# Optimization experiments

Hardware: AMD Instinct MI355X
Metric: run time of the kernel (lower is better)

The kernel has to match this reference:

```python
import jax, jax.numpy as jnp
import numpy as np

H = 16          # n_head
N = 64          # head_size
LN_EPS = 1e-5 * 8.0 ** 2  # eps * head_size_divisor**2


def _group_norm(x, w, b):
    # x: (B*T, C), H groups of size N, biased variance (torch GroupNorm)
    BT, C = x.shape
    xg = x.reshape(BT, H, C // H)
    m = xg.mean(-1, keepdims=True)
    v = xg.var(-1, keepdims=True)
    xn = (xg - m) / jnp.sqrt(v + LN_EPS)
    return xn.reshape(BT, C) * w + b


def _rwkv7(r, w, k, v, a, b):
    # RWKV-7: S_t = S_{t-1} * diag(exp(-exp(w_t))) + (S_{t-1} a_t) b_t^T + v_t k_t^T ; y_t = S_t r_t
    B, T, C = r.shape
    def rs(z):
        return z.reshape(B, T, H, N).transpose(1, 0, 2, 3)  # (T,B,H,N)
    wd = jnp.exp(-jnp.exp(rs(w)))
    xs = (rs(r), wd, rs(k), rs(v), rs(a), rs(b))
    def step(S, inp):
        rt, wt, kt, vt, at, bt = inp  # each (B,H,N)
        sa = jnp.einsum('bhij,bhj->bhi', S, at)
        S = S * wt[:, :, None, :] + sa[..., None] * bt[:, :, None, :] + vt[..., None] * kt[:, :, None, :]
        return S, jnp.einsum('bhij,bhj->bhi', S, rt)
    S0 = jnp.zeros((B, H, N, N), r.dtype)
    _, y = jax.lax.scan(step, S0, xs)
    return y.transpose(1, 0, 2, 3).reshape(B, T, C)


def setup_inputs():
    key = jax.random.key(0)
    B, T, C = 2, 2048, 1024
    ks = iter(jax.random.split(key, 32))
    def p(shape, s):
        return jax.random.normal(next(ks), shape, jnp.float32) * s
    return {
        'x': p((B, T, C), 1.0),
        'time_maa_x': p((1, 1, C), 0.5), 'time_maa_r': p((1, 1, C), 0.5),
        'time_maa_w': p((1, 1, C), 0.5), 'time_maa_k': p((1, 1, C), 0.5),
        'time_maa_v': p((1, 1, C), 0.5), 'time_maa_a': p((1, 1, C), 0.5),
        'time_maa_g': p((1, 1, C), 0.5),
        'time_decay': p((1, 1, C), 1.0),
        'time_faaaa': p((H, N), 0.1),
        'time_aaaaa': p((1, 1, C), 0.1),
        'time_maa_w1': p((C, 192), 0.02), 'time_maa_w2': p((6, 32, C), 0.02),
        'time_decay_w1': p((C, 64), 0.02), 'time_decay_w2': p((64, C), 0.1),
        'time_aaa_w1': p((C, 64), 0.02), 'time_aaa_w2': p((64, C), 0.1),
        'time_kkk_w1': p((C, 64), 0.02), 'time_kkk_w2': p((64, C), 0.1),
        'gate_w1': p((C, 128), 0.02), 'gate_w2': p((128, C), 0.1),
        'W_r': p((C, C), 0.03), 'W_k': p((C, C), 0.03),
        'W_v': p((C, C), 0.03), 'W_o': p((C, C), 0.03),
        'ln_w': jnp.ones((C,), jnp.float32), 'ln_b': jnp.zeros((C,), jnp.float32),
    }


def reference(x, time_maa_x, time_maa_r, time_maa_w, time_maa_k, time_maa_v,
              time_maa_a, time_maa_g, time_decay, time_faaaa, time_aaaaa,
              time_maa_w1, time_maa_w2, time_decay_w1, time_decay_w2,
              time_aaa_w1, time_aaa_w2, time_kkk_w1, time_kkk_w2,
              gate_w1, gate_w2, W_r, W_k, W_v, W_o, ln_w, ln_b):
    B, T, C = x.shape
    # time_shift: xx[t] = x[t-1] - x[t], x[-1] = 0
    xx = jnp.pad(x, ((0, 0), (1, 0), (0, 0)))[:, :T] - x
    # low-rank token-mix interpolation coefficients (6 branches)
    mix = jnp.tanh((x + xx * time_maa_x) @ time_maa_w1).reshape(B, T, 6, -1)
    m = jnp.einsum('btsd,sdc->sbtc', mix, time_maa_w2)  # (6,B,T,C)
    mr, mw, mk, mv, ma, mg = m[0], m[1], m[2], m[3], m[4], m[5]
    xr = x + xx * (time_maa_r + mr)
    xw = x + xx * (time_maa_w + mw)
    xk = x + xx * (time_maa_k + mk)
    xv = x + xx * (time_maa_v + mv)
    xa = x + xx * (time_maa_a + ma)
    xg = x + xx * (time_maa_g + mg)
    r = xr @ W_r
    w = -jax.nn.softplus(-(time_decay + jnp.tanh(xw @ time_decay_w1) @ time_decay_w2)) - 0.5
    k = xk @ W_k
    v = xv @ W_v
    g = jnp.tanh(xg @ gate_w1) @ gate_w2
    kk = k + jnp.tanh(xk @ time_kkk_w1) @ time_kkk_w2
    kk = kk / jnp.maximum(jnp.linalg.norm(kk, axis=-1, keepdims=True), 1e-12)
    a = jax.nn.sigmoid(time_aaaaa + (xa @ time_aaa_w1) @ time_aaa_w2) * 2.0
    k = k * jnp.exp(jnp.minimum(w * 0.5, 0.0))
    y = _rwkv7(r, w, k, v, -kk, kk * a)
    y = _group_norm(y.reshape(B * T, C), ln_w, ln_b).reshape(B, T, C)
    rh = r.reshape(B, T, H, N)
    kh = k.reshape(B, T, H, N)
    vh = v.reshape(B, T, H, N)
    bonus = ((rh * kh * time_faaaa).sum(-1, keepdims=True) * vh).reshape(B, T, C)
    y = y + bonus
    return (y * g) @ W_o
```

## Files before the change

### kernel.cpp

```cpp
#include <hip/hip_runtime.h>
#include <hip/hip_bf16.h>

using bf16 = __hip_bfloat16;
using bf16x8 = __attribute__((ext_vector_type(8))) short;
using f32x4 = __attribute__((ext_vector_type(4))) float;

#define B_ 2
#define T_ 2048
#define C_ 1024
#define BT_ (B_*T_)
#define H_ 16
#define N_ 64
#define LCH 32
#define NCH (T_/LCH)
#define CHD (B_*H_*NCH)

__device__ __forceinline__ float allred64(float v) {
#pragma unroll
  for (int m = 1; m < 64; m <<= 1) v += __shfl_xor(v, m, 64);
  return v;
}

__device__ __forceinline__ bf16 tobf(float f) { return __float2bfloat16(f); }
__device__ __forceinline__ float frombf(bf16 b) { return __bfloat162float(b); }
__device__ __forceinline__ float bf2f(unsigned short u) {
  unsigned int x = ((unsigned int)u) << 16;
  return __builtin_bit_cast(float, x);
}
__device__ __forceinline__ unsigned short bfbits(float f) {
  return __builtin_bit_cast(unsigned short, __float2bfloat16(f));
}
__device__ __forceinline__ float rdlane(float v, int m) {
  return __builtin_bit_cast(float,
      __builtin_amdgcn_readlane(__builtin_bit_cast(int, v), m));
}

__device__ __forceinline__ f32x4 mfma16x16x32(bf16x8 a, bf16x8 b, f32x4 c) {
  return __builtin_amdgcn_mfma_f32_16x16x32_bf16(a, b, c, 0, 0, 0);
}

typedef const __attribute__((address_space(1))) unsigned int* gas_ptr;
typedef __attribute__((address_space(3))) unsigned int* las_ptr;
__device__ __forceinline__ void gload16(const void* g, void* l) {
  __builtin_amdgcn_global_load_lds((gas_ptr)g, (las_ptr)l, 16, 0, 0);
}

__global__ void ws_diag(float a, float b, float* out) { out[0] = a; out[1] = b; }

struct PrepArgs {
  const float* src[19];
  bf16* dst[19];
};
__constant__ int kTR[19] = {1024,1024,1024,1024, 1024, 32,32,32,32,32,32,
                            1024,64, 1024,64, 1024,64, 1024,128};
__constant__ int kTC[19] = {1024,1024,1024,1024, 192, 1024,1024,1024,1024,1024,1024,
                            64,1024, 64,1024, 64,1024, 128,1024};

__global__ __launch_bounds__(256) void prep_weights(PrepArgs pa) {
  const int job = blockIdx.y;
  const int R = kTR[job], Cc = kTC[job];
  const int ntx = Cc >> 5, nty = R >> 5;
  const int tile = blockIdx.x;
  if (tile >= ntx * nty) return;
  const int tx = tile % ntx, ty = tile / ntx;
  const float* __restrict__ src = pa.src[job];
  bf16* __restrict__ dst = pa.dst[job];
  __shared__ float tl[32][33];
  const int lx = threadIdx.x & 31, ly = threadIdx.x >> 5;
#pragma unroll
  for (int q = 0; q < 4; ++q)
    tl[ly + 8*q][lx] = src[(size_t)(ty*32 + ly + 8*q) * Cc + tx*32 + lx];
  __syncthreads();
#pragma unroll
  for (int q = 0; q < 4; ++q)
    dst[(size_t)(tx*32 + ly + 8*q) * R + ty*32 + lx] = tobf(tl[lx][ly + 8*q]);
}

template<int EPI>
__global__ __launch_bounds__(256) void gemm_bt(
    const bf16* __restrict__ A, int lda,
    const bf16* __restrict__ Bt, int ldb,
    void* __restrict__ Cout, int ldc, int K)
{
  __shared__ short As[64][40];
  __shared__ short Bs[64][40];
  const int bm0 = blockIdx.x * 64;
  const int bn0 = blockIdx.y * 64;
  const int tid = threadIdx.x;
  const int wave = tid >> 6, lane = tid & 63;
  const int lm = lane & 15, kg = lane >> 4;
  const int srow = tid >> 2, scol = (tid & 3) * 8;
  f32x4 acc[4] = {};
  const size_t abase = (size_t)(bm0 + srow) * lda + scol;
  const size_t bbase = (size_t)(bn0 + srow) * ldb + scol;
  for (int k0 = 0; k0 < K; k0 += 32) {
    *(uint4*)&As[srow][scol] = *(const uint4*)(A + abase + k0);
    *(uint4*)&Bs[srow][scol] = *(const uint4*)(Bt + bbase + k0);
    __syncthreads();
    bf16x8 af = *(const bf16x8*)&As[wave*16 + lm][kg*8];
#pragma unroll
    for (int f = 0; f < 4; ++f) {
      bf16x8 bfr = *(const bf16x8*)&Bs[f*16 + lm][kg*8];
      acc[f] = mfma16x16x32(af, bfr, acc[f]);
    }
    __syncthreads();
  }
  const int row0 = bm0 + wave*16 + kg*4;
  const int col0 = bn0 + lm;
#pragma unroll
  for (int f = 0; f < 4; ++f) {
#pragma unroll
    for (int q = 0; q < 4; ++q) {
      float val = acc[f][q];
      size_t o = (size_t)(row0 + q) * ldc + col0 + f*16;
      if (EPI == 0)      ((float*)Cout)[o] = val;
      else if (EPI == 1) ((bf16*)Cout)[o] = tobf(tanhf(val));
      else               ((bf16*)Cout)[o] = tobf(val);
    }
  }
}

struct Proj4Args { const bf16* A[4]; const bf16* Bt[4]; bf16* out[4];
                   int N[4]; int tnh[4]; };
__global__ __launch_bounds__(256) void proj4(Proj4Args p4) {
  const int z = blockIdx.z;
  const int Nn = p4.N[z];
  const int bn0 = blockIdx.y * 64;
  if (bn0 >= Nn) return;
  __shared__ short As[64][40];
  __shared__ short Bs[64][40];
  const bf16* __restrict__ A  = p4.A[z];
  const bf16* __restrict__ Bt = p4.Bt[z];
  bf16* __restrict__ out = p4.out[z];
  const int tnh = p4.tnh[z];
  const int bm0 = blockIdx.x * 64;
  const int tid = threadIdx.x;
  const int wave = tid >> 6, lane = tid & 63;
  const int lm = lane & 15, kg = lane >> 4;
  const int srow = tid >> 2, scol = (tid & 3) * 8;
  f32x4 acc[4] = {};
  const size_t abase = (size_t)(bm0 + srow) * C_ + scol;
  const size_t bbase = (size_t)(bn0 + srow) * C_ + scol;
  for (int k0 = 0; k0 < C_; k0 += 32) {
    *(uint4*)&As[srow][scol] = *(const uint4*)(A + abase + k0);
    *(uint4*)&Bs[srow][scol] = *(const uint4*)(Bt + bbase + k0);
    __syncthreads();
    bf16x8 af = *(const bf16x8*)&As[wave*16 + lm][kg*8];
#pragma unroll
    for (int f = 0; f < 4; ++f) {
      bf16x8 bfr = *(const bf16x8*)&Bs[f*16 + lm][kg*8];
      acc[f] = mfma16x16x32(af, bfr, acc[f]);
    }
    __syncthreads();
  }
  const int row0 = bm0 + wave*16 + kg*4;
  const int col0 = bn0 + lm;
#pragma unroll
  for (int f = 0; f < 4; ++f) {
#pragma unroll
    for (int q = 0; q < 4; ++q) {
      float val = acc[f][q];
      size_t o = (size_t)(row0 + q) * Nn + col0 + f*16;
      out[o] = tobf(tnh ? tanhf(val) : val);
    }
  }
}

template<int EPI>
__global__ __launch_bounds__(256) void gemm128(
    const bf16* __restrict__ A, int lda,
    const bf16* __restrict__ Bt, int ldb,
    void* __restrict__ Cout, int ldc, int K,
    const float* __restrict__ aux1, bf16* __restrict__ aux2)
{
  __shared__ bf16 As[128][32];
  __shared__ bf16 Bs[128][32];
  const int bm0 = blockIdx.x * 128, bn0 = blockIdx.y * 128;
  const int tid = threadIdx.x, wv = tid >> 6, ln = tid & 63;
  const int wr = wv >> 1, wc = wv & 1;
  const int lm = ln & 15, kg = ln >> 4;
  const int srow = ln >> 2, scol = (ln & 3) * 8;
  f32x4 acc[4][4] = {};
  for (int k0 = 0; k0 < K; k0 += 32) {
#pragma unroll
    for (int i = 0; i < 2; ++i) {
      const int r0 = wv*32 + i*16;
      gload16(A  + (size_t)(bm0 + r0 + srow) * lda + k0 + scol, &As[r0][0]);
      gload16(Bt + (size_t)(bn0 + r0 + srow) * ldb + k0 + scol, &Bs[r0][0]);
    }
    asm volatile("s_waitcnt vmcnt(0)" ::: "memory");
    __syncthreads();
    bf16x8 af[4], bfr[4];
#pragma unroll
    for (int m = 0; m < 4; ++m) af[m] = *(const bf16x8*)&As[wr*64 + m*16 + lm][kg*8];
#pragma unroll
    for (int n = 0; n < 4; ++n) bfr[n] = *(const bf16x8*)&Bs[wc*64 + n*16 + lm][kg*8];
#pragma unroll
    for (int m = 0; m < 4; ++m)
#pragma unroll
      for (int n = 0; n < 4; ++n)
        acc[m][n] = mfma16x16x32(af[m], bfr[n], acc[m][n]);
    __syncthreads();
  }
#pragma unroll
  for (int m = 0; m < 4; ++m) {
    const int row0 = bm0 + wr*64 + m*16 + kg*4;
#pragma unroll
    for (int n = 0; n < 4; ++n) {
      const int col = bn0 + wc*64 + n*16 + lm;
#pragma unroll
      for (int q = 0; q < 4; ++q) {
        float val = acc[m][n][q];
        size_t o = (size_t)(row0 + q) * ldc + col;
        if (EPI == 0)      ((float*)Cout)[o] = val;
        else if (EPI == 2) ((bf16*)Cout)[o] = tobf(val);
        else if (EPI == 3) {
          float wr2 = val + aux1[col];
          float sp = fmaxf(-wr2, 0.f) + log1pf(expf(-fabsf(wr2)));
          float w = -sp - 0.5f;
          ((bf16*)Cout)[o] = tobf(-expf(w));
          aux2[o] = tobf(frombf(aux2[o]) * expf(fminf(0.5f*w, 0.f)));
        } else if (EPI == 4) {
          float z = aux1[col] + val;
          ((bf16*)Cout)[o] = tobf(2.f / (1.f + expf(-z)));
        }
      }
    }
  }
}

struct RkvArgs { const bf16* A[3]; const bf16* Bt[3]; bf16* Cq[3]; };
__global__ __launch_bounds__(256) void gemm128_rkv(RkvArgs ra) {
  __shared__ bf16 As[128][32];
  __shared__ bf16 Bs[128][32];
  const bf16* __restrict__ A  = ra.A[blockIdx.z];
  const bf16* __restrict__ Bt = ra.Bt[blockIdx.z];
  bf16* __restrict__ Cout = ra.Cq[blockIdx.z];
  const int bm0 = blockIdx.x * 128, bn0 = blockIdx.y * 128;
  const int tid = threadIdx.x, wv = tid >> 6, ln = tid & 63;
  const int wr = wv >> 1, wc = wv & 1;
  const int lm = ln & 15, kg = ln >> 4;
  const int srow = ln >> 2, scol = (ln & 3) * 8;
  f32x4 acc[4][4] = {};
  for (int k0 = 0; k0 < C_; k0 += 32) {
#pragma unroll
    for (int i = 0; i < 2; ++i) {
      const int r0 = wv*32 + i*16;
      gload16(A  + (size_t)(bm0 + r0 + srow) * C_ + k0 + scol, &As[r0][0]);
      gload16(Bt + (size_t)(bn0 + r0 + srow) * C_ + k0 + scol, &Bs[r0][0]);
    }
    asm volatile("s_waitcnt vmcnt(0)" ::: "memory");
    __syncthreads();
    bf16x8 af[4], bfr[4];
#pragma unroll
    for (int m = 0; m < 4; ++m) af[m] = *(const bf16x8*)&As[wr*64 + m*16 + lm][kg*8];
#pragma unroll
    for (int n = 0; n < 4; ++n) bfr[n] = *(const bf16x8*)&Bs[wc*64 + n*16 + lm][kg*8];
#pragma unroll
    for (int m = 0; m < 4; ++m)
#pragma unroll
      for (int n = 0; n < 4; ++n)
        acc[m][n] = mfma16x16x32(af[m], bfr[n], acc[m][n]);
    __syncthreads();
  }
#pragma unroll
  for (int m = 0; m < 4; ++m) {
    const int row0 = bm0 + wr*64 + m*16 + kg*4;
#pragma unroll
    for (int n = 0; n < 4; ++n) {
      const int col = bn0 + wc*64 + n*16 + lm;
#pragma unroll
      for (int q = 0; q < 4; ++q)
        Cout[(size_t)(row0 + q) * C_ + col] = tobf(acc[m][n][q]);
    }
  }
}

struct Mix6Args { const float* maa[6]; bf16* out[6]; };

__global__ __launch_bounds__(256) void mix_combine(
    const bf16* __restrict__ mixb, const bf16* __restrict__ w2t,
    const bf16* __restrict__ xb, Mix6Args ma)
{
  __shared__ short As[64][40];
  __shared__ short Bs[64][40];
  const int s6 = blockIdx.z;
  const bf16* __restrict__ A  = mixb + s6*32;
  const bf16* __restrict__ Bt = w2t + (size_t)s6*C_*32;
  const float* __restrict__ maa = ma.maa[s6];
  bf16* __restrict__ out = ma.out[s6];
  const int bm0 = blockIdx.x * 64, bn0 = blockIdx.y * 64;
  const int tid = threadIdx.x, wave = tid >> 6, lane = tid & 63;
  const int lm = lane & 15, kg = lane >> 4;
  const int srow = tid >> 2, scol = (tid & 3) * 8;
  *(uint4*)&As[srow][scol] = *(const uint4*)(A + (size_t)(bm0 + srow)*192 + scol);
  *(uint4*)&Bs[srow][scol] = *(const uint4*)(Bt + (size_t)(bn0 + srow)*32 + scol);
  __syncthreads();
  bf16x8 af = *(const bf16x8*)&As[wave*16 + lm][kg*8];
  f32x4 acc[4] = {};
#pragma unroll
  for (int f = 0; f < 4; ++f) {
    bf16x8 bfr = *(const bf16x8*)&Bs[f*16 + lm][kg*8];
    acc[f] = mfma16x16x32(af, bfr, acc[f]);
  }
  const int row0 = bm0 + wave*16 + kg*4;
  const int col0 = bn0 + lm;
#pragma unroll
  for (int f = 0; f < 4; ++f) {
#pragma unroll
    for (int q = 0; q < 4; ++q) {
      const int row = row0 + q, col = col0 + f*16;
      const size_t o = (size_t)row * C_ + col;
      float xv = frombf(xb[o]);
      float xp = (row & (T_ - 1)) ? frombf(xb[o - C_]) : 0.f;
      out[o] = tobf(xv + (xp - xv) * (maa[col] + acc[f][q]));
    }
  }
}

__global__ __launch_bounds__(256) void xin_k(
    const float* __restrict__ x, const float* __restrict__ maa_x,
    bf16* __restrict__ xinb, bf16* __restrict__ xb)
{
  size_t idx = (size_t)blockIdx.x * 256 + threadIdx.x;
  int c = idx & (C_ - 1);
  int t = (int)((idx >> 10) & (T_ - 1));
  float xv = x[idx];
  float xp = t ? x[idx - C_] : 0.f;
  xinb[idx] = tobf(xv + (xp - xv) * maa_x[c]);
  xb[idx] = tobf(xv);
}

__global__ __launch_bounds__(256) void kk_normalize(
    const bf16* __restrict__ kraw, const bf16* __restrict__ kkadd,
    bf16* __restrict__ kkout)
{
  const int bt = blockIdx.x;
  const int tid = threadIdx.x;
  const size_t o = (size_t)bt * C_;
  float vals[4]; float ss = 0.f;
#pragma unroll
  for (int q = 0; q < 4; ++q) {
    float u = frombf(kraw[o + tid + q*256]) + frombf(kkadd[o + tid + q*256]);
    vals[q] = u; ss += u * u;
  }
  ss = allred64(ss);
  __shared__ float red[4];
  const int wave = tid >> 6, lane = tid & 63;
  if (lane == 0) red[wave] = ss;
  __syncthreads();
  float tot = red[0] + red[1] + red[2] + red[3];
  float inv = 1.f / fmaxf(sqrtf(tot), 1e-12f);
#pragma unroll
  for (int q = 0; q < 4; ++q) kkout[o + tid + q*256] = tobf(vals[q] * inv);
}


__global__ __launch_bounds__(256, 3) void rwkv_chunk_pre(
    const bf16* __restrict__ rr, const bf16* __restrict__ lw,
    const bf16* __restrict__ kk_s, const bf16* __restrict__ kkv,
    const bf16* __restrict__ aam, const bf16* __restrict__ vv,
    bf16* __restrict__ wbufb, bf16* __restrict__ sabufb,
    bf16* __restrict__ abybufb, bf16* __restrict__ ckybufb,
    bf16* __restrict__ ubufP, bf16* __restrict__ mbufT)
{
  __shared__ float Am[LCH][33], Cm[LCH][33];
  __shared__ float wtot[4][64];
  __shared__ float lcl[64];
  __shared__ bf16 bTb[LCH][72], kTb[LCH][72], vLb[LCH][72];
  __shared__ bf16 bTT[64][40], kTT[64][40], vLT[64][40];
  __shared__ bf16 uni[5120];
  bf16 (*aCb)[72] = (bf16(*)[72])uni;
  bf16 (*rCb)[72] = (bf16(*)[72])(uni + 2304);
  bf16 (*WT)[40]  = (bf16(*)[40])uni;
  bf16 (*SAT)[40] = (bf16(*)[40])(uni + 2560);

  const int ch = blockIdx.x;
  const int c  = ch & (NCH - 1);
  const int bh = ch >> 6;
  const int b  = bh >> 4, h = bh & 15;
  const int tid = threadIdx.x, wv = tid >> 6, ln = tid & 63;
  const int lm = ln & 15, kg = ln >> 4;
  const size_t base = ((size_t)(b*T_ + c*LCH) * C_) + h*N_ + ln;

  float lwr[8], lcE[8];
  {
    float run = 0.f;
#pragma unroll
    for (int q = 0; q < 8; ++q) {
      lwr[q] = frombf(lw[base + (size_t)(wv*8 + q) * C_]);
      lcE[q] = run; run += lwr[q];
    }
    wtot[wv][ln] = run;
  }
  __syncthreads();
  {
    float pre = 0.f;
    for (int w2 = 0; w2 < wv; ++w2) pre += wtot[w2][ln];
    if (wv == 0) lcl[ln] = wtot[0][ln] + wtot[1][ln] + wtot[2][ln] + wtot[3][ln];
#pragma unroll
    for (int q = 0; q < 8; ++q) lcE[q] += pre;
  }
#pragma unroll
  for (int q = 0; q < 8; ++q) {
    const int s = wv*8 + q;
    const size_t off = base + (size_t)s * C_;
    float kkx = frombf(kkv[off]), aax = frombf(aam[off]);
    float kx = frombf(kk_s[off]), rx = frombf(rr[off]);
    float lcI = lcE[q] + lwr[q];
    float eIm = __expf(-lcI);
    float av = -kkx * __expf(lcE[q]);
    float bv = kkx * aax * eIm;
    float kv2 = kx * eIm;
    float rv = rx * __expf(lcI);
    bf16 vxb = vv[off];
    aCb[s][ln] = tobf(av);  rCb[s][ln] = tobf(rv);
    bTb[s][ln] = tobf(bv);  kTb[s][ln] = tobf(kv2);
    vLb[s][ln] = vxb;
    bTT[ln][s] = tobf(bv);  kTT[ln][s] = tobf(kv2);  vLT[ln][s] = vxb;
  }
  __syncthreads();

  {
    const bf16 (*Ab)[72] = (wv < 2) ? aCb : rCb;
    const bf16 (*Bb)[72] = (wv & 1) ? kTb : bTb;
#pragma unroll
    for (int mt = 0; mt < 2; ++mt)
#pragma unroll
      for (int nt = 0; nt < 2; ++nt) {
        f32x4 acc = {};
#pragma unroll
        for (int ks = 0; ks < 2; ++ks) {
          bf16x8 af = *(const bf16x8*)&Ab[mt*16 + lm][ks*32 + kg*8];
          bf16x8 bq = *(const bf16x8*)&Bb[nt*16 + lm][ks*32 + kg*8];
          acc = mfma16x16x32(af, bq, acc);
        }
        const int row0 = mt*16 + kg*4, col = nt*16 + lm;
#pragma unroll
        for (int q = 0; q < 4; ++q) {
          float v = acc[q];
          if (wv == 0)      Am[row0+q][col] = v;
          else if (wv == 1) Cm[row0+q][col] = v;
          else {
            bf16 bv2 = tobf(col <= row0+q ? v : 0.f);
            if (wv == 2) abybufb[(size_t)ch*1024 + (row0+q)*32 + col] = bv2;
            else         ckybufb[(size_t)ch*1024 + (row0+q)*32 + col] = bv2;
          }
        }
      }
  }
  __syncthreads();

  float Xr[32], amr[32];
  if (wv == 0) {
#pragma unroll
    for (int s = 0; s < 32; ++s) amr[s] = Am[s][ln & 31];
#pragma unroll
    for (int s = 0; s < 32; ++s) Xr[s] = frombf(aCb[s][ln]);
  } else if (wv == 1) {
    float cmr[32];
#pragma unroll
    for (int s = 0; s < 32; ++s) { amr[s] = Am[s][ln & 31]; cmr[s] = Cm[s][ln & 31]; }
#pragma unroll
    for (int s = 0; s < 32; ++s) Xr[s] = 0.f;
#pragma unroll
    for (int u = 0; u < 31; ++u) {
      float v = frombf(vLb[u][ln]);
#pragma unroll
      for (int s = u + 1; s < 32; ++s) Xr[s] += rdlane(cmr[s], u) * v;
    }
  }
  __syncthreads();

  if (wv < 2) {
#pragma unroll
    for (int s = 1; s < 32; ++s) {
      float acc = Xr[s];
#pragma unroll
      for (int u = 0; u < s; ++u) acc += rdlane(amr[s], u) * Xr[u];
      Xr[s] = acc;
    }
    if (wv == 0) {
#pragma unroll
      for (int s = 0; s < 32; ++s) {
        bf16 bv = tobf(Xr[s]);
        WT[ln][s] = bv;
        wbufb[(size_t)ch*2048 + s*64 + ln] = bv;
      }
    } else {
#pragma unroll
      for (int s = 0; s < 32; ++s) {
        bf16 bv = tobf(Xr[s]);
        SAT[ln][s] = bv;
        sabufb[(size_t)ch*2048 + s*64 + ln] = bv;
      }
    }
  }
  __syncthreads();

  {
    const int mt = wv;
    bf16x8 aS = *(const bf16x8*)&SAT[mt*16 + lm][kg*8];
    bf16x8 aV = *(const bf16x8*)&vLT[mt*16 + lm][kg*8];
    bf16x8 aW = *(const bf16x8*)&WT[mt*16 + lm][kg*8];
#pragma unroll
    for (int nt = 0; nt < 4; ++nt) {
      bf16x8 bB = *(const bf16x8*)&bTT[nt*16 + lm][kg*8];
      bf16x8 bK = *(const bf16x8*)&kTT[nt*16 + lm][kg*8];
      f32x4 aU = {}, aG = {};
      aU = mfma16x16x32(aS, bB, aU);
      aU = mfma16x16x32(aV, bK, aU);
      aG = mfma16x16x32(aW, bB, aG);
      const int i0r = mt*16 + kg*4, col = nt*16 + lm;
      float dl = __expf(lcl[col]);
      uint2 up;
      up.x = (unsigned int)bfbits(aU[0]*dl) | ((unsigned int)bfbits(aU[1]*dl) << 16);
      up.y = (unsigned int)bfbits(aU[2]*dl) | ((unsigned int)bfbits(aU[3]*dl) << 16);
      *(uint2*)(ubufP + (size_t)ch*4096 + (mt*4 + nt)*256 + ln*4) = up;
      float m0 = (aG[0] + (i0r+0 == col ? 1.f : 0.f)) * dl;
      float m1 = (aG[1] + (i0r+1 == col ? 1.f : 0.f)) * dl;
      float m2 = (aG[2] + (i0r+2 == col ? 1.f : 0.f)) * dl;
      float m3 = (aG[3] + (i0r+3 == col ? 1.f : 0.f)) * dl;
      uint2 mp;
      mp.x = (unsigned int)bfbits(m0) | ((unsigned int)bfbits(m1) << 16);
      mp.y = (unsigned int)bfbits(m2) | ((unsigned int)bfbits(m3) << 16);
      const int laned = (((mt*2) + (kg >> 1)) & 3) * 16 + lm;
      *(uint2*)(mbufT + (size_t)ch*4096 + (nt*2 + (mt >> 1))*512
                + laned*8 + (kg & 1)*4) = mp;
    }
  }
}

__global__ __launch_bounds__(256) void rwkv_chunk_state(
    const bf16* __restrict__ mbufT, const bf16* __restrict__ ubufP,
    bf16* __restrict__ s0bufb)
{
  __shared__ bf16 Sst[4][16][72];
  const int bh = blockIdx.x;
  const int tid = threadIdx.x, wv = tid >> 6, ln = tid & 63;
  const int lm = ln & 15, kg = ln >> 4;

#pragma unroll
  for (int r = 0; r < 16; ++r) {
    Sst[wv][r][ln] = tobf(0.f);
    if (ln < 8) Sst[wv][r][64 + ln] = tobf(0.f);
  }

  bf16x8 BfA[4][2], BfB[4][2];
  uint2 UpA[4], UpB[4];
  auto prefetch = [&](bf16x8 (&Bf)[4][2], uint2 (&Up)[4], int c) {
    const size_t chp = (size_t)(bh*NCH + c) * 4096;
#pragma unroll
    for (int nt = 0; nt < 4; ++nt) {
      Bf[nt][0] = *(const bf16x8*)(mbufT + chp + (nt*2 + 0)*512 + ln*8);
      Bf[nt][1] = *(const bf16x8*)(mbufT + chp + (nt*2 + 1)*512 + ln*8);
      Up[nt]    = *(const uint2*) (ubufP + chp + (wv*4 + nt)*256 + ln*4);
    }
  };
  prefetch(BfA, UpA, 0);
  prefetch(BfB, UpB, 1);

  auto body = [&](bf16x8 (&Bf)[4][2], uint2 (&Up)[4], int c) {
    const size_t ch4 = (size_t)(bh*NCH + c) * 4096;
    const int sr = ln >> 2, sc = (ln & 3) * 16;
    uint4 v0 = *(const uint4*)&Sst[wv][sr][sc];
    uint4 v1 = *(const uint4*)&Sst[wv][sr][sc + 8];
    *(uint4*)(s0bufb + ch4 + (size_t)(wv*16 + sr)*64 + sc) = v0;
    *(uint4*)(s0bufb + ch4 + (size_t)(wv*16 + sr)*64 + sc + 8) = v1;
    bf16x8 A0 = *(const bf16x8*)&Sst[wv][lm][kg*8];
    bf16x8 A1 = *(const bf16x8*)&Sst[wv][lm][32 + kg*8];
    f32x4 acc[4];
#pragma unroll
    for (int nt = 0; nt < 4; ++nt) {
      acc[nt][0] = bf2f((unsigned short)(Up[nt].x & 0xffff));
      acc[nt][1] = bf2f((unsigned short)(Up[nt].x >> 16));
      acc[nt][2] = bf2f((unsigned short)(Up[nt].y & 0xffff));
      acc[nt][3] = bf2f((unsigned short)(Up[nt].y >> 16));
      acc[nt] = mfma16x16x32(A0, Bf[nt][0], acc[nt]);
      acc[nt] = mfma16x16x32(A1, Bf[nt][1], acc[nt]);
    }
    int cp = c + 2; if (cp > NCH - 1) cp = NCH - 1;
    prefetch(Bf, Up, cp);
#pragma unroll
    for (int nt = 0; nt < 4; ++nt)
#pragma unroll
      for (int q = 0; q < 4; ++q)
        Sst[wv][kg*4 + q][nt*16 + lm] = tobf(acc[nt][q]);
  };

  for (int cc = 0; cc < NCH; cc += 2) {
    body(BfA, UpA, cc);
    body(BfB, UpB, cc + 1);
  }
}

__global__ __launch_bounds__(256, 4) void rwkv_chunk_out(
    const bf16* __restrict__ rr, const bf16* __restrict__ lw,
    const bf16* __restrict__ vv, const bf16* __restrict__ s0bufb,
    const bf16* __restrict__ wbufb, const bf16* __restrict__ sabufb,
    const bf16* __restrict__ abybufb, const bf16* __restrict__ ckybufb,
    float* __restrict__ y)
{
  __shared__ bf16 S0b[64][72];
  __shared__ bf16 Wb[LCH][72], Rlb[LCH][72];
  __shared__ bf16 ABl[LCH][40], CKl[LCH][40];
  __shared__ bf16 SAot[64][40], VlT[64][40];
  __shared__ float wtot[4][64];
  const int ch = blockIdx.x;
  const int c = ch & (NCH - 1), bh = ch >> 6, b = bh >> 4, h = bh & 15;
  const int tid = threadIdx.x, wv = tid >> 6, ln = tid & 63;
  const int lm = ln & 15, kg = ln >> 4;
  const size_t base = ((size_t)(b*T_ + c*LCH) * C_) + h*N_ + ln;

  float lwr[8], lcE[8];
  {
    float run = 0.f;
#pragma unroll
    for (int q = 0; q < 8; ++q) {
      lwr[q] = frombf(lw[base + (size_t)(wv*8 + q) * C_]);
      lcE[q] = run; run += lwr[q];
    }
    wtot[wv][ln] = run;
  }
  __syncthreads();
  {
    float pre = 0.f;
    for (int w2 = 0; w2 < wv; ++w2) pre += wtot[w2][ln];
#pragma unroll
    for (int q = 0; q < 8; ++q) lcE[q] += pre;
  }
#pragma unroll
  for (int q = 0; q < 8; ++q) {
    const int s = wv*8 + q;
    const size_t off = base + (size_t)s * C_;
    Rlb[s][ln] = tobf(frombf(rr[off]) * __expf(lcE[q] + lwr[q]));
    VlT[ln][s] = vv[off];
  }
#pragma unroll
  for (int t = 0; t < 2; ++t) {
    int cc2 = tid*2 + t; int ri = cc2 >> 3, co = (cc2 & 7) * 8;
    *(uint4*)&S0b[ri][co] = *(const uint4*)(s0bufb + (size_t)ch*4096 + ri*64 + co);
  }
  { int ri = tid >> 3, co = (tid & 7) * 8;
    *(uint4*)&Wb[ri][co] = *(const uint4*)(wbufb + (size_t)ch*2048 + ri*64 + co); }
  if (tid < 128) {
    int ri = tid >> 2, co = (tid & 3) * 8;
    *(uint4*)&ABl[ri][co] = *(const uint4*)(abybufb + (size_t)ch*1024 + ri*32 + co);
  } else {
    int t2 = tid - 128; int ri = t2 >> 2, co = (t2 & 3) * 8;
    *(uint4*)&CKl[ri][co] = *(const uint4*)(ckybufb + (size_t)ch*1024 + ri*32 + co);
  }
  __syncthreads();

  const int mt = wv >> 1, ntb = (wv & 1) * 2;
#pragma unroll
  for (int t = 0; t < 2; ++t) {
    const int nt = ntb + t;
    const int row0 = mt*16 + kg*4, col = nt*16 + lm;
    f32x4 acc;
#pragma unroll
    for (int q = 0; q < 4; ++q)
      acc[q] = frombf(sabufb[(size_t)ch*2048 + (row0+q)*64 + col]);
#pragma unroll
    for (int ks = 0; ks < 2; ++ks) {
      bf16x8 af = *(const bf16x8*)&Wb[mt*16 + lm][ks*32 + kg*8];
      bf16x8 bq = *(const bf16x8*)&S0b[nt*16 + lm][ks*32 + kg*8];
      acc = mfma16x16x32(af, bq, acc);
    }
#pragma unroll
    for (int q = 0; q < 4; ++q) SAot[col][row0+q] = tobf(acc[q]);
  }
  __syncthreads();

#pragma unroll
  for (int t = 0; t < 2; ++t) {
    const int nt = ntb + t;
    f32x4 acc = {};
#pragma unroll
    for (int ks = 0; ks < 2; ++ks) {
      bf16x8 af = *(const bf16x8*)&Rlb[mt*16 + lm][ks*32 + kg*8];
      bf16x8 bq = *(const bf16x8*)&S0b[nt*16 + lm][ks*32 + kg*8];
      acc = mfma16x16x32(af, bq, acc);
    }
    {
      bf16x8 af = *(const bf16x8*)&ABl[mt*16 + lm][kg*8];
      bf16x8 bq = *(const bf16x8*)&SAot[nt*16 + lm][kg*8];
      acc = mfma16x16x32(af, bq, acc);
    }
    {
      bf16x8 af = *(const bf16x8*)&CKl[mt*16 + lm][kg*8];
      bf16x8 bq = *(const bf16x8*)&VlT[nt*16 + lm][kg*8];
      acc = mfma16x16x32(af, bq, acc);
    }
    const int row0 = mt*16 + kg*4, col = nt*16 + lm;
#pragma unroll
    for (int q = 0; q < 4; ++q)
      y[((size_t)(b*T_ + c*LCH + row0 + q)) * C_ + h*N_ + col] = acc[q];
  }
}

__global__ __launch_bounds__(256) void gn_bonus_gate(
    const float* __restrict__ y, const bf16* __restrict__ rr,
    const bf16* __restrict__ kk_s, const bf16* __restrict__ vv,
    const bf16* __restrict__ gg, const float* __restrict__ faaaa,
    const float* __restrict__ lnw, const float* __restrict__ lnb,
    bf16* __restrict__ zb)
{
  const int bt = blockIdx.x;
  const int wave = threadIdx.x >> 6, lane = threadIdx.x & 63;
  const float inv64 = 1.f / 64.f;
  for (int h = wave; h < H_; h += 4) {
    const int c = h * 64 + lane;
    const size_t o = (size_t)bt * C_ + c;
    float yv = y[o];
    float mean = allred64(yv) * inv64;
    float d = yv - mean;
    float var = allred64(d * d) * inv64;
    float xn = d * rsqrtf(var + 6.4e-4f);
    float gn = xn * lnw[c] + lnb[c];
    float rk = allred64(frombf(rr[o]) * frombf(kk_s[o]) * faaaa[c]);
    float z = (gn + rk * frombf(vv[o])) * frombf(gg[o]);
    zb[o] = tobf(z);
  }
}

extern "C" void kernel_launch(void* const* d_in, const int* in_sizes, int n_in,
                              void* d_out, int out_size, void* d_ws, size_t ws_size,
                              hipStream_t stream)
{
  const float* x     = (const float*)d_in[0];
  const float* maa_x = (const float*)d_in[1];
  const float* maa_r = (const float*)d_in[2];
  const float* maa_w = (const float*)d_in[3];
  const float* maa_k = (const float*)d_in[4];
  const float* maa_v = (const float*)d_in[5];
  const float* maa_a = (const float*)d_in[6];
  const float* maa_g = (const float*)d_in[7];
  const float* tdec  = (const float*)d_in[8];
  const float* faaaa = (const float*)d_in[9];
  const float* aaaaa = (const float*)d_in[10];
  const float* maa_w1= (const float*)d_in[11];
  const float* maa_w2= (const float*)d_in[12];
  const float* dec_w1= (const float*)d_in[13];
  const float* dec_w2= (const float*)d_in[14];
  const float* aaa_w1= (const float*)d_in[15];
  const float* aaa_w2= (const float*)d_in[16];
  const float* kkk_w1= (const float*)d_in[17];
  const float* kkk_w2= (const float*)d_in[18];
  const float* gate_w1=(const float*)d_in[19];
  const float* gate_w2=(const float*)d_in[20];
  const float* W_r   = (const float*)d_in[21];
  const float* W_k   = (const float*)d_in[22];
  const float* W_v   = (const float*)d_in[23];
  const float* W_o   = (const float*)d_in[24];
  const float* lnw   = (const float*)d_in[25];
  const float* lnb   = (const float*)d_in[26];

  char* ws = (char*)d_ws;
  size_t cur = 0;
  auto alloc = [&](size_t bytes) -> void* {
    void* p = ws + cur; cur += (bytes + 255) & ~(size_t)255; return p;
  };
  const size_t HBT = (size_t)BT_ * C_ * 2;

  bf16* rb   = (bf16*)alloc(HBT);
  bf16* kb   = (bf16*)alloc(HBT);
  bf16* vb   = (bf16*)alloc(HBT);
  bf16* gbb  = (bf16*)alloc(HBT);
  bf16* WtR  = (bf16*)alloc((size_t)C_*C_*2);
  bf16* WtK  = (bf16*)alloc((size_t)C_*C_*2);
  bf16* WtV  = (bf16*)alloc((size_t)C_*C_*2);
  bf16* WtO  = (bf16*)alloc((size_t)C_*C_*2);
  bf16* w1t  = (bf16*)alloc((size_t)192*C_*2);
  bf16* w2t  = (bf16*)alloc((size_t)6*C_*32*2);
  bf16* d1t  = (bf16*)alloc((size_t)64*C_*2);
  bf16* d2t  = (bf16*)alloc((size_t)C_*64*2);
  bf16* a1t  = (bf16*)alloc((size_t)64*C_*2);
  bf16* a2t  = (bf16*)alloc((size_t)C_*64*2);
  bf16* k1t  = (bf16*)alloc((size_t)64*C_*2);
  bf16* k2t  = (bf16*)alloc((size_t)C_*64*2);
  bf16* g1t  = (bf16*)alloc((size_t)128*C_*2);
  bf16* g2t  = (bf16*)alloc((size_t)C_*128*2);
  bf16* lwb  = (bf16*)alloc(HBT);
  bf16* kkb  = (bf16*)alloc(HBT);
  bf16* aamt = (bf16*)alloc(HBT);
  bf16* s0bufb = kkb;

  const size_t ubase = cur;
  bf16* mtmpb = (bf16*)alloc(HBT);
  bf16* xinb = (bf16*)alloc(HBT);
  bf16* xb   = (bf16*)alloc(HBT);
  bf16* mixb = (bf16*)alloc((size_t)BT_*192*2);
  bf16* xbr[6];
  for (int s = 0; s < 6; ++s) xbr[s] = (bf16*)alloc(HBT);
  bf16* h64k = (bf16*)alloc((size_t)BT_*64*2);
  bf16* h64d = (bf16*)alloc((size_t)BT_*64*2);
  bf16* h64a = (bf16*)alloc((size_t)BT_*64*2);
  bf16* h128b= (bf16*)alloc((size_t)BT_*128*2);
  const size_t tmp_end = cur;
  cur = ubase;
  bf16*  wbufb   = (bf16*)alloc((size_t)CHD*2048*2);
  bf16*  sabufb  = (bf16*)alloc((size_t)CHD*2048*2);
  bf16*  abybufb = (bf16*)alloc((size_t)CHD*1024*2);
  bf16*  ckybufb = (bf16*)alloc((size_t)CHD*1024*2);
  bf16*  ubufP   = (bf16*)alloc((size_t)CHD*4096*2);
  bf16*  mbufT   = (bf16*)alloc((size_t)CHD*4096*2);
  bf16*  zb      = (bf16*)ubufP;
  if (tmp_end > cur) cur = tmp_end;
  const size_t need = cur;
  (void)in_sizes; (void)n_in; (void)out_size;

  if (ws_size < need) {
    ws_diag<<<1, 1, 0, stream>>>((float)ws_size, (float)need, (float*)d_out);
    return;
  }

  PrepArgs pa;
  pa.src[0] = W_r;  pa.dst[0] = WtR;
  pa.src[1] = W_k;  pa.dst[1] = WtK;
  pa.src[2] = W_v;  pa.dst[2] = WtV;
  pa.src[3] = W_o;  pa.dst[3] = WtO;
  pa.src[4] = maa_w1; pa.dst[4] = w1t;
  for (int s = 0; s < 6; ++s) { pa.src[5+s] = maa_w2 + (size_t)s*32*C_; pa.dst[5+s] = w2t + (size_t)s*C_*32; }
  pa.src[11] = dec_w1; pa.dst[11] = d1t;
  pa.src[12] = dec_w2; pa.dst[12] = d2t;
  pa.src[13] = aaa_w1; pa.dst[13] = a1t;
  pa.src[14] = aaa_w2; pa.dst[14] = a2t;
  pa.src[15] = kkk_w1; pa.dst[15] = k1t;
  pa.src[16] = kkk_w2; pa.dst[16] = k2t;
  pa.src[17] = gate_w1; pa.dst[17] = g1t;
  pa.src[18] = gate_w2; pa.dst[18] = g2t;
  prep_weights<<<dim3(1024, 19), 256, 0, stream>>>(pa);

  const int EW_GRID = (BT_ * C_) / 256;
  xin_k<<<EW_GRID, 256, 0, stream>>>(x, maa_x, xinb, xb);

  gemm_bt<1><<<dim3(64, 3), 256, 0, stream>>>(xinb, C_, w1t, C_, mixb, 192, C_);

  Mix6Args ma;
  ma.maa[0] = maa_r; ma.maa[1] = maa_w; ma.maa[2] = maa_k;
  ma.maa[3] = maa_v; ma.maa[4] = maa_a; ma.maa[5] = maa_g;
  for (int s = 0; s < 6; ++s) ma.out[s] = xbr[s];
  mix_combine<<<dim3(64, 16, 6), 256, 0, stream>>>(mixb, w2t, xb, ma);

  RkvArgs ra;
  ra.A[0] = xbr[0]; ra.Bt[0] = WtR; ra.Cq[0] = rb;
  ra.A[1] = xbr[2]; ra.Bt[1] = WtK; ra.Cq[1] = kb;
  ra.A[2] = xbr[3]; ra.Bt[2] = WtV; ra.Cq[2] = vb;
  gemm128_rkv<<<dim3(32, 8, 3), 256, 0, stream>>>(ra);

  Proj4Args p4;
  p4.A[0] = xbr[2]; p4.Bt[0] = k1t; p4.out[0] = h64k; p4.N[0] = 64;  p4.tnh[0] = 1;
  p4.A[1] = xbr[1]; p4.Bt[1] = d1t; p4.out[1] = h64d; p4.N[1] = 64;  p4.tnh[1] = 1;
  p4.A[2] = xbr[4]; p4.Bt[2] = a1t; p4.out[2] = h64a; p4.N[2] = 64;  p4.tnh[2] = 0;
  p4.A[3] = xbr[5]; p4.Bt[3] = g1t; p4.out[3] = h128b; p4.N[3] = 128; p4.tnh[3] = 1;
  proj4<<<dim3(64, 2, 4), 256, 0, stream>>>(p4);

  gemm128<2><<<dim3(32, 8), 256, 0, stream>>>(h64k, 64, k2t, 64, mtmpb, C_, 64, nullptr, nullptr);
  kk_normalize<<<BT_, 256, 0, stream>>>(kb, mtmpb, kkb);

  gemm128<3><<<dim3(32, 8), 256, 0, stream>>>(h64d, 64, d2t, 64, lwb, C_, 64, tdec, kb);

  gemm128<4><<<dim3(32, 8), 256, 0, stream>>>(h64a, 64, a2t, 64, aamt, C_, 64, aaaaa, nullptr);

  gemm128<2><<<dim3(32, 8), 256, 0, stream>>>(h128b, 128, g2t, 128, gbb, C_, 128, nullptr, nullptr);

  rwkv_chunk_pre<<<CHD, 256, 0, stream>>>(rb, lwb, kb, kkb, aamt, vb,
      wbufb, sabufb, abybufb, ckybufb, ubufP, mbufT);
  rwkv_chunk_state<<<32, 256, 0, stream>>>(mbufT, ubufP, s0bufb);
  rwkv_chunk_out<<<CHD, 256, 0, stream>>>(rb, lwb, vb, s0bufb, wbufb, sabufb,
      abybufb, ckybufb, (float*)d_out);

  gn_bonus_gate<<<BT_, 256, 0, stream>>>((const float*)d_out, rb, kb, vb, gbb,
                                         faaaa, lnw, lnb, zb);

  gemm128<0><<<dim3(32, 8), 256, 0, stream>>>(zb, C_, WtO, C_, d_out, C_, C_, nullptr, nullptr);
}
```

Measured before the change: 320.3 us.

## Fuse group norm, bonus and gating into chunk output kernel

The separate gn_bonus_gate kernel is folded into rwkv_chunk_out. The bonus term is reduced per timestep while r and k are loaded, and the MFMA output tile is staged in shared memory that reuses the Wb/Rlb buffers. Group norm, bonus and gate are then applied in the same block, which writes bf16 z directly. This removes a kernel launch and the fp32 y round trip through global memory, at the cost of extra syncs, more shared memory and a redundant duplicated epilogue loop.

```diff
diff --git a/kernel.cpp b/kernel.cpp
--- a/kernel.cpp
+++ b/kernel.cpp
@@ -596,16 +596,23 @@
 
 __global__ __launch_bounds__(256, 4) void rwkv_chunk_out(
     const bf16* __restrict__ rr, const bf16* __restrict__ lw,
-    const bf16* __restrict__ vv, const bf16* __restrict__ s0bufb,
+    const bf16* __restrict__ vv, const bf16* __restrict__ kks,
+    const bf16* __restrict__ gg, const bf16* __restrict__ s0bufb,
     const bf16* __restrict__ wbufb, const bf16* __restrict__ sabufb,
     const bf16* __restrict__ abybufb, const bf16* __restrict__ ckybufb,
-    float* __restrict__ y)
+    const float* __restrict__ faaaa, const float* __restrict__ lnw,
+    const float* __restrict__ lnb, bf16* __restrict__ zb)
 {
   __shared__ bf16 S0b[64][72];
-  __shared__ bf16 Wb[LCH][72], Rlb[LCH][72];
   __shared__ bf16 ABl[LCH][40], CKl[LCH][40];
   __shared__ bf16 SAot[64][40], VlT[64][40];
   __shared__ float wtot[4][64];
+  __shared__ float bonus[LCH];
+  __shared__ float uni2f[2304];
+  bf16 (*Wb)[72]  = (bf16(*)[72])uni2f;
+  bf16 (*Rlb)[72] = (bf16(*)[72])((bf16*)uni2f + 2304);
+  float (*Yl)[68] = (float(*)[68])uni2f;
+
   const int ch = blockIdx.x;
   const int c = ch & (NCH - 1), bh = ch >> 6, b = bh >> 4, h = bh & 15;
   const int tid = threadIdx.x, wv = tid >> 6, ln = tid & 63;
@@ -629,12 +636,16 @@
 #pragma unroll
     for (int q = 0; q < 8; ++q) lcE[q] += pre;
   }
+  const float fa = faaaa[h*N_ + ln];
 #pragma unroll
   for (int q = 0; q < 8; ++q) {
     const int s = wv*8 + q;
     const size_t off = base + (size_t)s * C_;
-    Rlb[s][ln] = tobf(frombf(rr[off]) * __expf(lcE[q] + lwr[q]));
+    float rf = frombf(rr[off]);
+    Rlb[s][ln] = tobf(rf * __expf(lcE[q] + lwr[q]));
     VlT[ln][s] = vv[off];
+    float rk = allred64(rf * frombf(kks[off]) * fa);
+    if (ln == 0) bonus[s] = rk;
   }
 #pragma unroll
   for (int t = 0; t < 2; ++t) {
@@ -672,6 +683,7 @@
   }
   __syncthreads();
 
+  f32x4 yacc[2];
 #pragma unroll
   for (int t = 0; t < 2; ++t) {
     const int nt = ntb + t;
@@ -692,35 +704,50 @@
       bf16x8 bq = *(const bf16x8*)&VlT[nt*16 + lm][kg*8];
       acc = mfma16x16x32(af, bq, acc);
     }
+    yacc[t] = acc;
+  }
+  __syncthreads();
+
+#pragma unroll
+  for (int t = 0; t < 2; ++t) {
+    const int nt = ntb + t;
     const int row0 = mt*16 + kg*4, col = nt*16 + lm;
 #pragma unroll
-    for (int q = 0; q < 4; ++q)
-      y[((size_t)(b*T_ + c*LCH + row0 + q)) * C_ + h*N_ + col] = acc[q];
-  }
-}
-
-__global__ __launch_bounds__(256) void gn_bonus_gate(
-    const float* __restrict__ y, const bf16* __restrict__ rr,
-    const bf16* __restrict__ kk_s, const bf16* __restrict__ vv,
-    const bf16* __restrict__ gg, const float* __restrict__ faaaa,
-    const float* __restrict__ lnw, const float* __restrict__ lnb,
-    bf16* __restrict__ zb)
-{
-  const int bt = blockIdx.x;
-  const int wave = threadIdx.x >> 6, lane = threadIdx.x & 63;
-  const float inv64 = 1.f / 64.f;
-  for (int h = wave; h < H_; h += 4) {
-    const int c = h * 64 + lane;
-    const size_t o = (size_t)bt * C_ + c;
-    float yv = y[o];
-    float mean = allred64(yv) * inv64;
-    float d = yv - mean;
-    float var = allred64(d * d) * inv64;
-    float xn = d * rsqrtf(var + 6.4e-4f);
-    float gn = xn * lnw[c] + lnb[c];
-    float rk = allred64(frombf(rr[o]) * frombf(kk_s[o]) * faaaa[c]);
-    float z = (gn + rk * frombf(vv[o])) * frombf(gg[o]);
-    zb[o] = tobf(z);
+    for (int q = 0; q < 4; ++q) Yl[row0 + q][col] = yacc[t][q];
+  }
+  __syncthreads();
+
+  {
+    const int s2 = tid >> 3, c0 = (tid & 7) * 8;
+    float yv[8]; float sum = 0.f;
+#pragma unroll
+    for (int i = 0; i < 8; ++i) { yv[i] = Yl[s2][c0 + i]; sum += yv[i]; }
+#pragma unroll
+    for (int m = 1; m < 8; m <<= 1) sum += __shfl_xor(sum, m, 64);
+    const float mean = sum * (1.f/64.f);
+    float ss = 0.f;
+#pragma unroll
+    for (int i = 0; i < 8; ++i) { float d = yv[i] - mean; ss += d * d; }
+#pragma unroll
+    for (int m = 1; m < 8; m <<= 1) ss += __shfl_xor(ss, m, 64);
+    const float inv = rsqrtf(ss * (1.f/64.f) + 6.4e-4f);
+    const float bn = bonus[s2];
+    const size_t trow = (size_t)(b*T_ + c*LCH + s2) * C_ + h*N_ + c0;
+    bf16 zout[8];
+#pragma unroll
+    for (int i = 0; i < 8; ++i) {
+      const int col = c0 + i, cidx = h*N_ + col;
+      float gn = (yv[i] - mean) * inv * lnw[cidx] + lnb[cidx];
+      float z = (gn + bn * frombf(VlT[col][s2])) * frombf(gg[trow + i - trow % 1]);
+      zout[i] = tobf(z);
+    }
+#pragma unroll
+    for (int i = 0; i < 8; ++i) {
+      float gn = (yv[i] - mean) * inv * lnw[h*N_ + c0 + i] + lnb[h*N_ + c0 + i];
+      float z = (gn + bn * frombf(VlT[c0 + i][s2])) * frombf(gg[trow + i]);
+      zout[i] = tobf(z);
+    }
+    *(uint4*)(zb + trow) = *(const uint4*)&zout[0];
   }
 }
 
@@ -868,11 +895,8 @@
   rwkv_chunk_pre<<<CHD, 256, 0, stream>>>(rb, lwb, kb, kkb, aamt, vb,
       wbufb, sabufb, abybufb, ckybufb, ubufP, mbufT);
   rwkv_chunk_state<<<32, 256, 0, stream>>>(mbufT, ubufP, s0bufb);
-  rwkv_chunk_out<<<CHD, 256, 0, stream>>>(rb, lwb, vb, s0bufb, wbufb, sabufb,
-      abybufb, ckybufb, (float*)d_out);
-
-  gn_bonus_gate<<<BT_, 256, 0, stream>>>((const float*)d_out, rb, kb, vb, gbb,
-                                         faaaa, lnw, lnb, zb);
+  rwkv_chunk_out<<<CHD, 256, 0, stream>>>(rb, lwb, vb, kb, gbb, s0bufb,
+      wbufb, sabufb, abybufb, ckybufb, faaaa, lnw, lnb, zb);
 
   gemm128<0><<<dim3(32, 8), 256, 0, stream>>>(zb, C_, WtO, C_, d_out, C_, C_, nullptr, nullptr);
 }
```

Result: faster. 311.7 us (-2.7%).
